# Performance work log

Measured on AMD Instinct MI355X. Metric: run time of the kernel, lower is better.

The kernel has to match this reference:

```python
import jax, jax.numpy as jnp
import numpy as np

# TT factorization: vocab = 8*8*8*8*16 = 65536, dim = 4^5 = 1024, rank 16
SHAPE = [(8, 4), (8, 4), (8, 4), (8, 4), (16, 4)]
RANKS = [1, 16, 16, 16, 16, 1]
VOCAB = 65536
DIM = 1024
BATCH, SEQ = 8, 2048


def setup_inputs() -> dict:
    key = jax.random.key(0)
    ks = jax.random.split(key, len(SHAPE) + 1)
    inp = {}
    for k, (n, m) in enumerate(SHAPE):
        core = jax.random.normal(ks[k], (RANKS[k], n * m, RANKS[k + 1]), dtype=jnp.float32) * 0.01
        inp[f"core{k}"] = core
    inp["indices"] = jax.random.randint(ks[-1], (BATCH, SEQ), 0, VOCAB)
    return inp


def _tt_full(cores):
    # Faithful port of tt_to_matrix: chain matmul of cores, then a flat reshape
    # to (VOCAB, DIM).  (The original code reshapes merged_shape -> (rows, cols)
    # directly, without the inverse interleave permute; we replicate that.)
    result = cores[0]  # (1, n0*m0, r1)
    for core in cores[1:]:
        r_prev = result.shape[-1]
        result = (result.reshape(-1, r_prev) @ core.reshape(r_prev, -1))
        result = result.reshape(1, -1, core.shape[-1])
    return result.reshape(VOCAB, DIM)


def reference(core0, core1, core2, core3, core4, indices):
    full = _tt_full([core0, core1, core2, core3, core4])  # (VOCAB, DIM)
    return jnp.take(full, indices, axis=0)              # (BATCH, SEQ, DIM)
```

## Files before the change

kernel.cpp:

```cpp
#include <hip/hip_runtime.h>
#include <hip/hip_bf16.h>


typedef float f32x4 __attribute__((ext_vector_type(4)));

#define RSTRIDE 20
#define GSTRIDE 328

__global__ __launch_bounds__(256) void tt_embed_kernel(
    const float* __restrict__ c0,
    const float* __restrict__ c1,
    const float* __restrict__ c2,
    const float* __restrict__ c3,
    const float* __restrict__ c4,
    const int*   __restrict__ idx,
    float*       __restrict__ out,
    int n_tokens)
{
    const int t   = threadIdx.x;
    const int tl  = t >> 5;
    const int l32 = t & 31;
    const int r   = t & 15;
    const int l   = t & 63;
    const int wid = t >> 6;
    const int token = blockIdx.x * 8 + tl;
    const int v = (token < n_tokens) ? idx[token] : 0;

    __shared__ float w4s[8 * GSTRIDE];
    __shared__ float w2b[8][20];
    __shared__ float w3b[8][20];

    float4 c4v[16];
    #pragma unroll
    for (int r4 = 0; r4 < 16; ++r4)
        c4v[r4] = *(const float4*)(c4 + (r4 << 6) + ((l & 15) << 2));

    {
        const int i0 = (v >> 11) & 31;
        const int i1 = (v >> 6) & 31;
        float w2r = 0.f;
        #pragma unroll
        for (int r1 = 0; r1 < 16; ++r1)
            w2r = fmaf(c0[i0 * 16 + r1], c1[(r1 * 32 + i1) * 16 + r], w2r);
        w2b[tl][r] = w2r;
    }

    float4 w2v[4];
    #pragma unroll
    for (int q = 0; q < 4; ++q)
        w2v[q] = *(const float4*)&w2b[tl][q << 2];

    {
        const int i2 = (v >> 1) & 31;
        float w3r = 0.f;
        #pragma unroll
        for (int q = 0; q < 4; ++q) {
            w3r = fmaf(w2v[q].x, c2[((q * 4 + 0) * 32 + i2) * 16 + r], w3r);
            w3r = fmaf(w2v[q].y, c2[((q * 4 + 1) * 32 + i2) * 16 + r], w3r);
            w3r = fmaf(w2v[q].z, c2[((q * 4 + 2) * 32 + i2) * 16 + r], w3r);
            w3r = fmaf(w2v[q].w, c2[((q * 4 + 3) * 32 + i2) * 16 + r], w3r);
        }
        w3b[tl][r] = w3r;
    }

    float4 w3v[4];
    #pragma unroll
    for (int q = 0; q < 4; ++q)
        w3v[q] = *(const float4*)&w3b[tl][q << 2];

    {
        const int vlow16 = (v & 1) << 4;
        float4 a0 = {0,0,0,0}, a1 = {0,0,0,0};
        const float wv_arr0[16] = {w3v[0].x, w3v[0].y, w3v[0].z, w3v[0].w,
                                   w3v[1].x, w3v[1].y, w3v[1].z, w3v[1].w,
                                   w3v[2].x, w3v[2].y, w3v[2].z, w3v[2].w,
                                   w3v[3].x, w3v[3].y, w3v[3].z, w3v[3].w};
        #pragma unroll
        for (int r3 = 0; r3 < 16; ++r3) {
            const float wv = wv_arr0[r3];
            const float* base = c3 + ((r3 * 32 + vlow16) << 4);
            const float4 b0 = *(const float4*)(base + (l32 << 2));
            const float4 b1 = *(const float4*)(base + 128 + (l32 << 2));
            a0.x = fmaf(wv, b0.x, a0.x); a0.y = fmaf(wv, b0.y, a0.y);
            a0.z = fmaf(wv, b0.z, a0.z); a0.w = fmaf(wv, b0.w, a0.w);
            a1.x = fmaf(wv, b1.x, a1.x); a1.y = fmaf(wv, b1.y, a1.y);
            a1.z = fmaf(wv, b1.z, a1.z); a1.w = fmaf(wv, b1.w, a1.w);
        }
        float* sb = &w4s[tl * GSTRIDE + ((l32 & 3) << 2)];
        *(float4*)(sb + ((l32 >> 2)    ) * RSTRIDE) = a0;
        *(float4*)(sb + (8 + (l32 >> 2)) * RSTRIDE) = a1;
    }

    #pragma unroll
    for (int s = 0; s < 2; ++s) {
        const int slot = 2 * wid + s;
        const int tok  = blockIdx.x * 8 + slot;
        const float* slab = &w4s[slot * GSTRIDE];
        const int sub = l >> 4;
        const int colb = (l & 15) << 2;

        #pragma unroll
        for (int j = 0; j < 4; ++j) {
            const int row = (j << 2) + sub;
            const float* rp = slab + row * RSTRIDE;
            const float4 wa = *(const float4*)(rp);
            const float4 wb = *(const float4*)(rp + 4);
            const float4 wc = *(const float4*)(rp + 8);
            const float4 wd = *(const float4*)(rp + 12);

            float4 acc = {0,0,0,0};
            #define FMA4(WV, k)                          \
                acc.x = fmaf(WV, c4v[k].x, acc.x);       \
                acc.y = fmaf(WV, c4v[k].y, acc.y);       \
                acc.z = fmaf(WV, c4v[k].z, acc.z);       \
                acc.w = fmaf(WV, c4v[k].w, acc.w);
            FMA4(wa.x,  0) FMA4(wa.y,  1) FMA4(wa.z,  2) FMA4(wa.w,  3)
            FMA4(wb.x,  4) FMA4(wb.y,  5) FMA4(wb.z,  6) FMA4(wb.w,  7)
            FMA4(wc.x,  8) FMA4(wc.y,  9) FMA4(wc.z, 10) FMA4(wc.w, 11)
            FMA4(wd.x, 12) FMA4(wd.y, 13) FMA4(wd.z, 14) FMA4(wd.w, 15)
            #undef FMA4

            if (tok < n_tokens)
                __builtin_nontemporal_store(*(const f32x4*)&acc,
                    (f32x4*)(out + (size_t)tok * 1024 + (row << 6) + colb));
        }
    }
}

extern "C" void kernel_launch(void* const* d_in, const int* in_sizes, int n_in,
                              void* d_out, int out_size, void* d_ws, size_t ws_size,
                              hipStream_t stream) {
    const float* c0  = (const float*)d_in[0];
    const float* c1  = (const float*)d_in[1];
    const float* c2  = (const float*)d_in[2];
    const float* c3  = (const float*)d_in[3];
    const float* c4  = (const float*)d_in[4];
    const int*   idx = (const int*)d_in[5];
    float* out = (float*)d_out;

    const int n_tokens = in_sizes[5];
    const int grid = (n_tokens + 7) / 8;
    tt_embed_kernel<<<grid, 256, 0, stream>>>(c0, c1, c2, c3, c4, idx, out, n_tokens);
}
```

Measured before the change: 25.59 us.

## Split into three kernels with precombined c3*c4 matrix and bf16 MFMA expansion

Precomputes the contraction of core3 with core4 into a 1024x32 bf16 matrix laid out in MFMA fragment order, computes per-token rank-16 w3 vectors in a separate kernel (placed into a 32-wide zero-padded bf16 vector chosen by the low index bit), then expands each token with 16x16x32 bf16 MFMA instructions. This moves the dominant per-token FMA work onto matrix cores and removes the per-token recomputation of the c3 contraction. It adds two extra kernel launches plus a workspace round-trip, and drops precision from fp32 to bf16 on both operands, which risks tolerance failures. The fused kernel is kept as a fallback when the workspace is too small.

```diff
diff --git a/kernel.cpp b/kernel.cpp
--- a/kernel.cpp
+++ b/kernel.cpp
@@ -3,19 +3,131 @@
 
 
 typedef float f32x4 __attribute__((ext_vector_type(4)));
+typedef short bf16x8 __attribute__((ext_vector_type(8)));
+typedef short s16x4 __attribute__((ext_vector_type(4)));
+
+static __device__ __forceinline__ unsigned short f2bf(float x) {
+    __hip_bfloat16 h = __float2bfloat16(x);
+    return *reinterpret_cast<unsigned short*>(&h);
+}
+
+__global__ __launch_bounds__(256) void tt_mfrag(
+    const float* __restrict__ c3,
+    const float* __restrict__ c4,
+    unsigned short* __restrict__ mfrag)
+{
+    const int tid  = blockIdx.x * 256 + threadIdx.x;
+    const int tile = tid >> 9;
+    const int lane = (tid >> 3) & 63;
+    const int i    = tid & 7;
+    const int k = 4 * (lane >> 4) + (i & 3) + ((i >> 2) << 4);
+    const int d = (tile << 4) + (lane & 15);
+    const int r3 = k & 15;
+    const int b  = k >> 4;
+    const int i3 = (b << 4) + (d >> 6);
+    const int i4 = d & 63;
+    float acc = 0.f;
+    #pragma unroll
+    for (int r4 = 0; r4 < 16; ++r4)
+        acc = fmaf(c3[(r3 * 32 + i3) * 16 + r4], c4[(r4 << 6) + i4], acc);
+    mfrag[tid] = f2bf(acc);
+}
+
+__global__ __launch_bounds__(256) void tt_w3(
+    const float* __restrict__ c0, const float* __restrict__ c1,
+    const float* __restrict__ c2, const int* __restrict__ idx,
+    unsigned int* __restrict__ w3x, int n_tokens)
+{
+    const int t = threadIdx.x;
+    const int tl = t >> 4;
+    const int r  = t & 15;
+    const int token = blockIdx.x * 16 + tl;
+    const int v = (token < n_tokens) ? idx[token] : 0;
+
+    __shared__ float w2b[16][20];
+    __shared__ float w3b[16][20];
+
+    {
+        const int i0 = (v >> 11) & 31;
+        const int i1 = (v >> 6) & 31;
+        float w2r = 0.f;
+        #pragma unroll
+        for (int r1 = 0; r1 < 16; ++r1)
+            w2r = fmaf(c0[i0 * 16 + r1], c1[(r1 * 32 + i1) * 16 + r], w2r);
+        w2b[tl][r] = w2r;
+    }
+    float4 w2v[4];
+    #pragma unroll
+    for (int q = 0; q < 4; ++q)
+        w2v[q] = *(const float4*)&w2b[tl][q << 2];
+
+    {
+        const int i2 = (v >> 1) & 31;
+        float w3r = 0.f;
+        #pragma unroll
+        for (int q = 0; q < 4; ++q) {
+            w3r = fmaf(w2v[q].x, c2[((q * 4 + 0) * 32 + i2) * 16 + r], w3r);
+            w3r = fmaf(w2v[q].y, c2[((q * 4 + 1) * 32 + i2) * 16 + r], w3r);
+            w3r = fmaf(w2v[q].z, c2[((q * 4 + 2) * 32 + i2) * 16 + r], w3r);
+            w3r = fmaf(w2v[q].w, c2[((q * 4 + 3) * 32 + i2) * 16 + r], w3r);
+        }
+        w3b[tl][r] = w3r;
+    }
+
+    {
+        const int vlow = v & 1;
+        const int k0 = 2 * r, k1 = 2 * r + 1;
+        const float f0 = w3b[tl][k0 & 15];
+        const float f1 = w3b[tl][k1 & 15];
+        const unsigned int lo = ((k0 >> 4) == vlow) ? f2bf(f0) : 0u;
+        const unsigned int hi = ((k1 >> 4) == vlow) ? f2bf(f1) : 0u;
+        if (token < n_tokens)
+            w3x[token * 16 + r] = lo | (hi << 16);
+    }
+}
+
+__global__ __launch_bounds__(256) void tt_expand(
+    const unsigned short* __restrict__ mfrag,
+    const unsigned short* __restrict__ w3x,
+    float* __restrict__ out, int n_tokens)
+{
+    const int t = threadIdx.x;
+    const int w = t >> 6;
+    const int l = t & 63;
+    const int col = l & 15;
+    const int g   = l >> 4;
+    const int tg  = blockIdx.x;
+
+    const int token = tg * 16 + col;
+    const int tokc  = (token < n_tokens) ? token : (n_tokens - 1);
+    const bool ok   = (token < n_tokens);
+
+    const unsigned short* wrow = w3x + (size_t)tokc * 32;
+    const s16x4 blo = *(const s16x4*)(wrow + 4 * g);
+    const s16x4 bhi = *(const s16x4*)(wrow + 16 + 4 * g);
+    const bf16x8 bf = {blo.x, blo.y, blo.z, blo.w, bhi.x, bhi.y, bhi.z, bhi.w};
+
+    float* outp = out + (size_t)token * 1024 + (g << 2);
+
+    #pragma unroll
+    for (int n = 0; n < 16; ++n) {
+        const int T = w * 16 + n;
+        const bf16x8 af = *(const bf16x8*)(mfrag + (size_t)T * 512 + l * 8);
+        f32x4 acc = {0.f, 0.f, 0.f, 0.f};
+        acc = __builtin_amdgcn_mfma_f32_16x16x32_bf16(af, bf, acc, 0, 0, 0);
+        if (ok)
+            __builtin_nontemporal_store(acc, (f32x4*)(outp + (T << 4)));
+    }
+}
 
 #define RSTRIDE 20
 #define GSTRIDE 328
 
-__global__ __launch_bounds__(256) void tt_embed_kernel(
-    const float* __restrict__ c0,
-    const float* __restrict__ c1,
-    const float* __restrict__ c2,
-    const float* __restrict__ c3,
-    const float* __restrict__ c4,
-    const int*   __restrict__ idx,
-    float*       __restrict__ out,
-    int n_tokens)
+__global__ __launch_bounds__(256) void tt_embed_fused(
+    const float* __restrict__ c0, const float* __restrict__ c1,
+    const float* __restrict__ c2, const float* __restrict__ c3,
+    const float* __restrict__ c4, const int* __restrict__ idx,
+    float* __restrict__ out, int n_tokens)
 {
     const int t   = threadIdx.x;
     const int tl  = t >> 5;
@@ -36,20 +148,17 @@
         c4v[r4] = *(const float4*)(c4 + (r4 << 6) + ((l & 15) << 2));
 
     {
-        const int i0 = (v >> 11) & 31;
-        const int i1 = (v >> 6) & 31;
+        const int i0 = (v >> 11) & 31, i1 = (v >> 6) & 31;
         float w2r = 0.f;
         #pragma unroll
         for (int r1 = 0; r1 < 16; ++r1)
             w2r = fmaf(c0[i0 * 16 + r1], c1[(r1 * 32 + i1) * 16 + r], w2r);
         w2b[tl][r] = w2r;
     }
-
     float4 w2v[4];
     #pragma unroll
     for (int q = 0; q < 4; ++q)
         w2v[q] = *(const float4*)&w2b[tl][q << 2];
-
     {
         const int i2 = (v >> 1) & 31;
         float w3r = 0.f;
@@ -62,12 +171,10 @@
         }
         w3b[tl][r] = w3r;
     }
-
     float4 w3v[4];
     #pragma unroll
     for (int q = 0; q < 4; ++q)
         w3v[q] = *(const float4*)&w3b[tl][q << 2];
-
     {
         const int vlow16 = (v & 1) << 4;
         float4 a0 = {0,0,0,0}, a1 = {0,0,0,0};
@@ -90,7 +197,6 @@
         *(float4*)(sb + ((l32 >> 2)    ) * RSTRIDE) = a0;
         *(float4*)(sb + (8 + (l32 >> 2)) * RSTRIDE) = a1;
     }
-
     #pragma unroll
     for (int s = 0; s < 2; ++s) {
         const int slot = 2 * wid + s;
@@ -98,7 +204,6 @@
         const float* slab = &w4s[slot * GSTRIDE];
         const int sub = l >> 4;
         const int colb = (l & 15) << 2;
-
         #pragma unroll
         for (int j = 0; j < 4; ++j) {
             const int row = (j << 2) + sub;
@@ -107,19 +212,17 @@
             const float4 wb = *(const float4*)(rp + 4);
             const float4 wc = *(const float4*)(rp + 8);
             const float4 wd = *(const float4*)(rp + 12);
-
             float4 acc = {0,0,0,0};
-            #define FMA4(WV, k)                          \
-                acc.x = fmaf(WV, c4v[k].x, acc.x);       \
-                acc.y = fmaf(WV, c4v[k].y, acc.y);       \
-                acc.z = fmaf(WV, c4v[k].z, acc.z);       \
-                acc.w = fmaf(WV, c4v[k].w, acc.w);
-            FMA4(wa.x,  0) FMA4(wa.y,  1) FMA4(wa.z,  2) FMA4(wa.w,  3)
-            FMA4(wb.x,  4) FMA4(wb.y,  5) FMA4(wb.z,  6) FMA4(wb.w,  7)
-            FMA4(wc.x,  8) FMA4(wc.y,  9) FMA4(wc.z, 10) FMA4(wc.w, 11)
-            FMA4(wd.x, 12) FMA4(wd.y, 13) FMA4(wd.z, 14) FMA4(wd.w, 15)
-            #undef FMA4
-
+            #define FB4(WV, K)                           \
+                acc.x = fmaf(WV, c4v[K].x, acc.x);       \
+                acc.y = fmaf(WV, c4v[K].y, acc.y);       \
+                acc.z = fmaf(WV, c4v[K].z, acc.z);       \
+                acc.w = fmaf(WV, c4v[K].w, acc.w);
+            FB4(wa.x,  0) FB4(wa.y,  1) FB4(wa.z,  2) FB4(wa.w,  3)
+            FB4(wb.x,  4) FB4(wb.y,  5) FB4(wb.z,  6) FB4(wb.w,  7)
+            FB4(wc.x,  8) FB4(wc.y,  9) FB4(wc.z, 10) FB4(wc.w, 11)
+            FB4(wd.x, 12) FB4(wd.y, 13) FB4(wd.z, 14) FB4(wd.w, 15)
+            #undef FB4
             if (tok < n_tokens)
                 __builtin_nontemporal_store(*(const f32x4*)&acc,
                     (f32x4*)(out + (size_t)tok * 1024 + (row << 6) + colb));
@@ -139,6 +242,19 @@
     float* out = (float*)d_out;
 
     const int n_tokens = in_sizes[5];
-    const int grid = (n_tokens + 7) / 8;
-    tt_embed_kernel<<<grid, 256, 0, stream>>>(c0, c1, c2, c3, c4, idx, out, n_tokens);
-}
+    const size_t ws_needed = 65536 + (size_t)n_tokens * 64 + 256;
+
+    if (ws_size >= ws_needed) {
+        unsigned short* mfrag = (unsigned short*)d_ws;
+        unsigned int*   w3x   = (unsigned int*)((char*)d_ws + 65536);
+        const int ngrp = (n_tokens + 15) / 16;
+        tt_mfrag<<<128, 256, 0, stream>>>(c3, c4, mfrag);
+        tt_w3<<<ngrp, 256, 0, stream>>>(c0, c1, c2, idx, w3x, n_tokens);
+        tt_expand<<<ngrp, 256, 0, stream>>>(mfrag, (const unsigned short*)w3x,
+                                            out, n_tokens);
+    } else {
+        const int grid = (n_tokens + 7) / 8;
+        tt_embed_fused<<<grid, 256, 0, stream>>>(c0, c1, c2, c3, c4, idx, out,
+                                                 n_tokens);
+    }
+}
```

Measured after the change: 32.14 us. 25.6% more time.
